# Performance work log

Measured on AMD Instinct MI355X. Metric: run time of the kernel, lower is better.

## Reference

```python
import jax, jax.numpy as jnp
import numpy as np

B, C_IN, N = 16, 64, 8192
C_OUT, NUM_RING = 128, 8
EPS = 1e-5  # BatchNorm1d default


def setup_inputs() -> dict:
    key = jax.random.key(0)
    k1, k2, k3, k4 = jax.random.split(key, 4)
    x = jax.random.normal(k1, (B, C_IN, N), dtype=jnp.float32)
    ring = jax.random.randint(k2, (B, N), 0, NUM_RING, dtype=jnp.int32)
    W = jax.random.normal(k3, (NUM_RING, C_OUT, C_IN), dtype=jnp.float32) * 0.05
    b = jax.random.normal(k4, (NUM_RING, C_OUT), dtype=jnp.float32) * 0.05
    gamma = jnp.ones((NUM_RING, C_OUT), dtype=jnp.float32)
    beta = jnp.zeros((NUM_RING, C_OUT), dtype=jnp.float32)
    return {"x": x, "ring": ring, "W": W, "b": b, "gamma": gamma, "beta": beta}


def reference(x, ring, W, b, gamma, beta):
    Bb, C, Nn = x.shape
    num_ring = W.shape[0]
    M = Bb * Nn
    xf = x.transpose(0, 2, 1).reshape(M, C)      # [M, 64] point features
    rf = ring.reshape(M)                          # [M] ring id per point

    # Per-ring Conv1d(64->128, k=1): linear with ring-selected weights.
    # num_ring is small; masked dense GEMMs avoid gathering [M,128,64] weights.
    y = jnp.zeros((M, W.shape[1]), dtype=xf.dtype)
    for r in range(num_ring):
        yr = xf @ W[r].T + b[r]
        y = jnp.where((rf == r)[:, None], yr, y)  # [M, 128]

    # Training-mode BatchNorm1d per ring group: stats over all points of that
    # ring across all batches (BN sees [1,128,M_r]). Biased variance.
    cnt = jax.ops.segment_sum(jnp.ones((M,), y.dtype), rf, num_segments=num_ring)
    cnt = jnp.maximum(cnt, 1.0)[:, None]          # [R,1]
    s = jax.ops.segment_sum(y, rf, num_segments=num_ring)       # [R,128]
    ss = jax.ops.segment_sum(y * y, rf, num_segments=num_ring)  # [R,128]
    mean = s / cnt
    var = ss / cnt - mean * mean
    yn = (y - mean[rf]) * jax.lax.rsqrt(var[rf] + EPS) * gamma[rf] + beta[rf]

    # Segment max over (batch, ring) pairs, broadcast back to every point.
    bidx = jnp.repeat(jnp.arange(Bb, dtype=rf.dtype), Nn)        # [M]
    seg = bidx * num_ring + rf
    mx = jax.ops.segment_max(yn, seg, num_segments=Bb * num_ring)  # [B*R,128]
    out = mx[seg].reshape(Bb, Nn, -1).transpose(0, 2, 1)         # [B,128,N]
    return out
```

## Files before the change

### kernel.cpp

```cpp
#include <hip/hip_runtime.h>
#include <stdint.h>
#include <math.h>

#define B_    16
#define CIN   64
#define NPT   8192
#define COUT  128
#define NRING 8
#define EPSV  1e-5f
#define CAP   2048u
#define MBLK  6

typedef unsigned int uint32;
typedef unsigned short ushort;
typedef unsigned long long ull;
typedef short short8 __attribute__((ext_vector_type(8)));
typedef float floatx4 __attribute__((ext_vector_type(4)));

__device__ __forceinline__ uint32 fkey(float f) {
  uint32 u = __float_as_uint(f);
  return (u & 0x80000000u) ? ~u : (u | 0x80000000u);
}
__device__ __forceinline__ float kinv(uint32 k) {
  uint32 u = (k & 0x80000000u) ? (k ^ 0x80000000u) : ~k;
  return __uint_as_float(u);
}
__device__ __forceinline__ uint32 f2bf(float f) {
  uint32 u = __float_as_uint(f);
  return (u + 0x7fffu + ((u >> 16) & 1u)) >> 16;
}

__global__ __launch_bounds__(256) void k_init(
    const float* __restrict__ W, ushort* __restrict__ Wb,
    uint32* __restrict__ cursor,
    float* __restrict__ sums, float* __restrict__ ssums,
    uint32* __restrict__ mxkey, uint32* __restrict__ mnkey)
{
  int tid = threadIdx.x;
  int blk = blockIdx.x;
  if (blk < 32) {
    int idx0 = blk * 256 + tid;
    for (int idx = idx0; idx < B_ * NRING * COUT; idx += 32 * 256) {
      mxkey[idx] = 0u;
      mnkey[idx] = 0xFFFFFFFFu;
      if (idx < NRING * COUT) { sums[idx] = 0.f; ssums[idx] = 0.f; }
      if (idx < B_ * NRING)   cursor[idx] = (uint32)idx * CAP;
    }
  } else {
    int idx0 = (blk - 32) * 256 + tid;
    for (int idx = idx0; idx < NRING * COUT * CIN; idx += 8 * 256)
      Wb[idx] = (ushort)f2bf(W[idx]);
  }
}

__global__ __launch_bounds__(256) void k_scatter(
    const float* __restrict__ x, const int* __restrict__ ring,
    uint32* __restrict__ cursor, ushort* __restrict__ xsb)
{
  __shared__ uint32 xl2[256 * 33];
  __shared__ int    dstrow[256];
  __shared__ ushort rankl[256];
  __shared__ uint32 wcnt[4][NRING], woff[4][NRING];
  __shared__ uint32 rbase[NRING], rstart[NRING];

  int tid  = threadIdx.x;
  int lane = tid & 63;
  int w    = tid >> 6;
  int blk  = blockIdx.x;
  int b    = blk >> 5;
  int n0   = (blk & 31) * 256;

  int rl = ring[b * NPT + n0 + tid];
  uint32 wrank = 0, mycnt = 0;
  #pragma unroll
  for (int rr = 0; rr < NRING; ++rr) {
    ull m = __ballot(rl == rr);
    if (rl == rr) wrank = (uint32)__popcll(m & ((1ull << lane) - 1ull));
    if (lane == rr) mycnt = (uint32)__popcll(m);
  }
  if (lane < NRING) wcnt[w][lane] = mycnt;
  __syncthreads();
  if (tid < NRING) {
    uint32 t = wcnt[0][tid] + wcnt[1][tid] + wcnt[2][tid] + wcnt[3][tid];
    rbase[tid] = atomicAdd(&cursor[b * NRING + tid], t);
  }
  if (tid == 0) {
    uint32 acc = 0;
    for (int rr = 0; rr < NRING; ++rr) {
      rstart[rr] = acc;
      uint32 o = acc;
      #pragma unroll
      for (int ww = 0; ww < 4; ++ww) { woff[ww][rr] = o; o += wcnt[ww][rr]; }
      acc = o;
    }
  }
  __syncthreads();
  int myrow = (int)(woff[w][rl] + wrank);
  rankl[tid] = (ushort)myrow;
  {
    uint32 gpos = rbase[rl] + ((uint32)myrow - rstart[rl]);
    uint32 limit = (uint32)(b * NRING + rl + 1) * CAP;
    dstrow[myrow] = (gpos < limit) ? (int)gpos : -1;
  }
  __syncthreads();

  int myr0 = rankl[lane * 4 + 0];
  int myr1 = rankl[lane * 4 + 1];
  int myr2 = rankl[lane * 4 + 2];
  int myr3 = rankl[lane * 4 + 3];
  const float* xb = x + (size_t)b * CIN * NPT + n0;
  #pragma unroll
  for (int kp = 0; kp < 8; ++kp) {
    int k0 = w * 16 + kp * 2;
    float4 va = *reinterpret_cast<const float4*>(xb + (size_t)k0 * NPT + lane * 4);
    float4 vb = *reinterpret_cast<const float4*>(xb + (size_t)(k0 + 1) * NPT + lane * 4);
    int idx = k0 >> 1;
    xl2[myr0 * 33 + idx] = f2bf(va.x) | (f2bf(vb.x) << 16);
    xl2[myr1 * 33 + idx] = f2bf(va.y) | (f2bf(vb.y) << 16);
    xl2[myr2 * 33 + idx] = f2bf(va.z) | (f2bf(vb.z) << 16);
    xl2[myr3 * 33 + idx] = f2bf(va.w) | (f2bf(vb.w) << 16);
  }
  __syncthreads();

  uint4* dst = reinterpret_cast<uint4*>(xsb);
  #pragma unroll
  for (int it = 0; it < 8; ++it) {
    int slot = tid + it * 256;
    int row = slot >> 3;
    int p   = slot & 7;
    int dr  = dstrow[row];
    if (dr >= 0) {
      uint4 v;
      v.x = xl2[row * 33 + 4 * p + 0];
      v.y = xl2[row * 33 + 4 * p + 1];
      v.z = xl2[row * 33 + 4 * p + 2];
      v.w = xl2[row * 33 + 4 * p + 3];
      dst[(size_t)dr * 8 + p] = v;
    }
  }
}

__global__ __launch_bounds__(256) void k_main(
    const ushort* __restrict__ xsb, const ushort* __restrict__ Wb,
    const uint32* __restrict__ cursor,
    float* __restrict__ sums, float* __restrict__ ssums,
    uint32* __restrict__ mxkey, uint32* __restrict__ mnkey)
{
  int blk = blockIdx.x;
  int c4 = blk % MBLK;
  int r  = (blk / MBLK) & 7;
  int b  = blk / (MBLK * NRING);
  uint32 segBase = (uint32)(b * NRING + r) * CAP;
  uint32 segCnt  = __builtin_amdgcn_readfirstlane(
                       min(cursor[b * NRING + r] - segBase, CAP));

  int tid = threadIdx.x;
  int lane = tid & 63;
  int w = tid >> 6;
  uint32 m0 = (uint32)(c4 * 4 + w) * 64;
  if (m0 >= segCnt) return;

  int lm = lane & 15;
  int lk = lane >> 4;

  const ushort* wr = Wb + (size_t)r * COUT * CIN;
  short8 bfr[8][2];
  #pragma unroll
  for (int nt = 0; nt < 8; ++nt) {
    const ushort* wc = wr + (size_t)(nt * 16 + lm) * CIN + lk * 8;
    bfr[nt][0] = *reinterpret_cast<const short8*>(wc);
    bfr[nt][1] = *reinterpret_cast<const short8*>(wc + 32);
  }

  float s_[8], ss_[8], mx_[8], mn_[8];
  #pragma unroll
  for (int nt = 0; nt < 8; ++nt) {
    s_[nt] = 0.f; ss_[nt] = 0.f;
    mx_[nt] = -__builtin_inff(); mn_[nt] = __builtin_inff();
  }

  #pragma unroll
  for (int mt = 0; mt < 4; ++mt) {
    uint32 row_rel = m0 + (uint32)mt * 16 + (uint32)lm;
    bool valid = row_rel < segCnt;
    uint32 row_g = segBase + (valid ? row_rel : (segCnt - 1));
    const ushort* xr = xsb + (size_t)row_g * CIN + lk * 8;
    short8 a0 = *reinterpret_cast<const short8*>(xr);
    short8 a1 = *reinterpret_cast<const short8*>(xr + 32);
    if (!valid) { a0 = (short8)0; a1 = (short8)0; }

    #pragma unroll
    for (int nt = 0; nt < 8; ++nt) {
      floatx4 f = {0.f, 0.f, 0.f, 0.f};
      f = __builtin_amdgcn_mfma_f32_16x16x32_bf16(a0, bfr[nt][0], f, 0, 0, 0);
      f = __builtin_amdgcn_mfma_f32_16x16x32_bf16(a1, bfr[nt][1], f, 0, 0, 0);
      #pragma unroll
      for (int j = 0; j < 4; ++j) {
        bool vj = (m0 + (uint32)mt * 16 + (uint32)(lk * 4 + j)) < segCnt;
        float zv = f[j];
        s_[nt] += zv;
        ss_[nt] = fmaf(zv, zv, ss_[nt]);
        mx_[nt] = fmaxf(mx_[nt], vj ? zv : -__builtin_inff());
        mn_[nt] = fminf(mn_[nt], vj ? zv :  __builtin_inff());
      }
    }
  }

  #pragma unroll
  for (int nt = 0; nt < 8; ++nt) {
    float sv = s_[nt], qv = ss_[nt], Mv = mx_[nt], mv = mn_[nt];
    sv += __shfl_xor(sv, 16, 64); sv += __shfl_xor(sv, 32, 64);
    qv += __shfl_xor(qv, 16, 64); qv += __shfl_xor(qv, 32, 64);
    Mv = fmaxf(Mv, __shfl_xor(Mv, 16, 64)); Mv = fmaxf(Mv, __shfl_xor(Mv, 32, 64));
    mv = fminf(mv, __shfl_xor(mv, 16, 64)); mv = fminf(mv, __shfl_xor(mv, 32, 64));
    if (lane < 16) {
      int ch = nt * 16 + lane;
      atomicAdd(&sums [r * COUT + ch], sv);
      atomicAdd(&ssums[r * COUT + ch], qv);
      atomicMax(&mxkey[(b * NRING + r) * COUT + ch], fkey(Mv));
      atomicMin(&mnkey[(b * NRING + r) * COUT + ch], fkey(mv));
    }
  }
}

__global__ __launch_bounds__(256) void k_bcast(
    const int* __restrict__ ring, const uint32* __restrict__ cursor,
    const float* __restrict__ sums, const float* __restrict__ ssums,
    const uint32* __restrict__ mxkey, const uint32* __restrict__ mnkey,
    const float* __restrict__ gamma, const float* __restrict__ beta,
    float* __restrict__ out)
{
  __shared__ float mxl[NRING * 129];
  __shared__ float ringcnt[NRING];
  int tid = threadIdx.x;
  int blk = blockIdx.x;
  int b   = blk >> 5;
  int n0  = (blk & 31) * 256;

  if (tid < NRING) {
    uint32 t = 0;
    for (int bb = 0; bb < B_; ++bb)
      t += min(cursor[bb * NRING + tid] - (uint32)(bb * NRING + tid) * CAP, CAP);
    ringcnt[tid] = fmaxf((float)t, 1.f);
  }
  __syncthreads();

  for (int j = tid; j < NRING * COUT; j += 256) {
    int r = j >> 7;
    float cnt  = ringcnt[r];
    float mean = sums[j] / cnt;
    float var  = fmaxf(ssums[j] / cnt - mean * mean, 0.f);
    float inv  = 1.f / sqrtf(var + EPSV);
    float a    = gamma[j] * inv;
    float bet  = beta[j];
    float zmax = kinv(mxkey[b * NRING * COUT + j]);
    float zmin = kinv(mnkey[b * NRING * COUT + j]);
    mxl[r * 129 + (j & 127)] = (a >= 0.f) ? fmaf(a, zmax - mean, bet)
                                          : fmaf(a, zmin - mean, bet);
  }
  __syncthreads();

  int wv = tid >> 6, lane = tid & 63;
  int nb = n0 + lane * 4;
  int4 r4 = *reinterpret_cast<const int4*>(&ring[b * NPT + nb]);
  int ro0 = r4.x * 129, ro1 = r4.y * 129, ro2 = r4.z * 129, ro3 = r4.w * 129;
  float* ob = out + (size_t)b * COUT * NPT + nb;
  #pragma unroll 8
  for (int c = wv * 32; c < wv * 32 + 32; ++c) {
    float4 v;
    v.x = mxl[ro0 + c];
    v.y = mxl[ro1 + c];
    v.z = mxl[ro2 + c];
    v.w = mxl[ro3 + c];
    *reinterpret_cast<float4*>(ob + (size_t)c * NPT) = v;
  }
}

extern "C" void kernel_launch(void* const* d_in, const int* in_sizes, int n_in,
                              void* d_out, int out_size, void* d_ws, size_t ws_size,
                              hipStream_t stream)
{
  const float* x     = (const float*)d_in[0];
  const int*   ring  = (const int*)  d_in[1];
  const float* W     = (const float*)d_in[2];
  const float* gamma = (const float*)d_in[4];
  const float* beta  = (const float*)d_in[5];
  float* out = (float*)d_out;

  ushort* Wb      = (ushort*)d_ws;
  uint32* cursor  = (uint32*)(Wb + 65536);
  float*  sums    = (float*)(cursor + 128);
  float*  ssums   = sums + 1024;
  uint32* mxkey   = (uint32*)(ssums + 1024);
  uint32* mnkey   = mxkey + 16384;

  ushort* xsb = (ushort*)out;

  k_init   <<<dim3(40),  dim3(256), 0, stream>>>(W, Wb, cursor, sums, ssums, mxkey, mnkey);
  k_scatter<<<dim3(512), dim3(256), 0, stream>>>(x, ring, cursor, xsb);
  k_main   <<<dim3(B_ * NRING * MBLK), dim3(256), 0, stream>>>(xsb, Wb, cursor, sums, ssums, mxkey, mnkey);
  k_bcast  <<<dim3(512), dim3(256), 0, stream>>>(ring, cursor, sums, ssums, mxkey, mnkey, gamma, beta, out);
}
```

Baseline: 77.59 us.

## Fuse scatter and per-ring GEMM into one kernel using LDS-local ring grouping

Merges the scatter and GEMM kernels: each 128-point block sorts its points by ring in LDS into 16-row padded tiles, then each wave runs the MFMA GEMM for two rings straight from LDS. This drops the global bf16 staging buffer, the per-segment cursors and their capacity cap, and one kernel launch. Statistics atomics are spread over 8 slots to reduce contention, and the broadcast kernel sums those slots. In exchange, every block reloads the weights for all rings and has padding waste in small per-ring groups, and many more atomics are issued overall.

Result: slower. 148.7 us (+91.6%).

```diff
diff --git a/kernel.cpp b/kernel.cpp
--- a/kernel.cpp
+++ b/kernel.cpp
@@ -8,8 +8,6 @@
 #define COUT  128
 #define NRING 8
 #define EPSV  1e-5f
-#define CAP   2048u
-#define MBLK  6
 
 typedef unsigned int uint32;
 typedef unsigned short ushort;
@@ -32,8 +30,8 @@
 
 __global__ __launch_bounds__(256) void k_init(
     const float* __restrict__ W, ushort* __restrict__ Wb,
-    uint32* __restrict__ cursor,
-    float* __restrict__ sums, float* __restrict__ ssums,
+    float* __restrict__ sums8, float* __restrict__ ssums8,
+    uint32* __restrict__ ringtot8,
     uint32* __restrict__ mxkey, uint32* __restrict__ mnkey)
 {
   int tid = threadIdx.x;
@@ -43,8 +41,8 @@
     for (int idx = idx0; idx < B_ * NRING * COUT; idx += 32 * 256) {
       mxkey[idx] = 0u;
       mnkey[idx] = 0xFFFFFFFFu;
-      if (idx < NRING * COUT) { sums[idx] = 0.f; ssums[idx] = 0.f; }
-      if (idx < B_ * NRING)   cursor[idx] = (uint32)idx * CAP;
+      if (idx < NRING * COUT * 8) { sums8[idx] = 0.f; ssums8[idx] = 0.f; }
+      if (idx < NRING * 8)        ringtot8[idx] = 0u;
     }
   } else {
     int idx0 = (blk - 32) * 256 + tid;
@@ -53,179 +51,149 @@
   }
 }
 
-__global__ __launch_bounds__(256) void k_scatter(
+__global__ __launch_bounds__(256, 3) void k_fused(
     const float* __restrict__ x, const int* __restrict__ ring,
-    uint32* __restrict__ cursor, ushort* __restrict__ xsb)
-{
-  __shared__ uint32 xl2[256 * 33];
-  __shared__ int    dstrow[256];
-  __shared__ ushort rankl[256];
-  __shared__ uint32 wcnt[4][NRING], woff[4][NRING];
-  __shared__ uint32 rbase[NRING], rstart[NRING];
+    const ushort* __restrict__ Wb,
+    float* __restrict__ sums8, float* __restrict__ ssums8,
+    uint32* __restrict__ ringtot8,
+    uint32* __restrict__ mxkey, uint32* __restrict__ mnkey)
+{
+  __shared__ uint32 xlf[256 * 32];
+  __shared__ ushort slotl[128];
+  __shared__ uint32 wcnt[2][NRING];
+  __shared__ uint32 gsize[NRING], astart[NRING];
 
   int tid  = threadIdx.x;
   int lane = tid & 63;
   int w    = tid >> 6;
   int blk  = blockIdx.x;
-  int b    = blk >> 5;
-  int n0   = (blk & 31) * 256;
-
-  int rl = ring[b * NPT + n0 + tid];
-  uint32 wrank = 0, mycnt = 0;
-  #pragma unroll
-  for (int rr = 0; rr < NRING; ++rr) {
-    ull m = __ballot(rl == rr);
-    if (rl == rr) wrank = (uint32)__popcll(m & ((1ull << lane) - 1ull));
-    if (lane == rr) mycnt = (uint32)__popcll(m);
-  }
-  if (lane < NRING) wcnt[w][lane] = mycnt;
-  __syncthreads();
-  if (tid < NRING) {
-    uint32 t = wcnt[0][tid] + wcnt[1][tid] + wcnt[2][tid] + wcnt[3][tid];
-    rbase[tid] = atomicAdd(&cursor[b * NRING + tid], t);
-  }
+  int b    = blk >> 6;
+  int n0   = (blk & 63) * 128;
+
+  {
+    uint4* z4 = reinterpret_cast<uint4*>(xlf);
+    #pragma unroll
+    for (int i = 0; i < 8; ++i) z4[tid + i * 256] = make_uint4(0u, 0u, 0u, 0u);
+  }
+
+  int rl = 0; uint32 wrank = 0;
+  if (tid < 128) {
+    rl = ring[b * NPT + n0 + tid];
+    #pragma unroll
+    for (int rr = 0; rr < NRING; ++rr) {
+      ull m = __ballot(rl == rr);
+      if (rl == rr) wrank = (uint32)__popcll(m & ((1ull << lane) - 1ull));
+      if (lane == rr) wcnt[w][rr] = (uint32)__popcll(m);
+    }
+  }
+  __syncthreads();
   if (tid == 0) {
-    uint32 acc = 0;
-    for (int rr = 0; rr < NRING; ++rr) {
-      rstart[rr] = acc;
-      uint32 o = acc;
-      #pragma unroll
-      for (int ww = 0; ww < 4; ++ww) { woff[ww][rr] = o; o += wcnt[ww][rr]; }
-      acc = o;
-    }
-  }
-  __syncthreads();
-  int myrow = (int)(woff[w][rl] + wrank);
-  rankl[tid] = (ushort)myrow;
+    uint32 a = 0;
+    #pragma unroll
+    for (int r = 0; r < NRING; ++r) {
+      astart[r] = a;
+      uint32 g = wcnt[0][r] + wcnt[1][r];
+      gsize[r] = g;
+      a = (a + g + 15u) & ~15u;
+    }
+  }
+  __syncthreads();
+  if (tid < 128)
+    slotl[tid] = (ushort)(astart[rl] + (w ? wcnt[0][rl] : 0u) + wrank);
+  __syncthreads();
+
   {
-    uint32 gpos = rbase[rl] + ((uint32)myrow - rstart[rl]);
-    uint32 limit = (uint32)(b * NRING + rl + 1) * CAP;
-    dstrow[myrow] = (gpos < limit) ? (int)gpos : -1;
-  }
-  __syncthreads();
-
-  int myr0 = rankl[lane * 4 + 0];
-  int myr1 = rankl[lane * 4 + 1];
-  int myr2 = rankl[lane * 4 + 2];
-  int myr3 = rankl[lane * 4 + 3];
-  const float* xb = x + (size_t)b * CIN * NPT + n0;
-  #pragma unroll
-  for (int kp = 0; kp < 8; ++kp) {
-    int k0 = w * 16 + kp * 2;
-    float4 va = *reinterpret_cast<const float4*>(xb + (size_t)k0 * NPT + lane * 4);
-    float4 vb = *reinterpret_cast<const float4*>(xb + (size_t)(k0 + 1) * NPT + lane * 4);
-    int idx = k0 >> 1;
-    xl2[myr0 * 33 + idx] = f2bf(va.x) | (f2bf(vb.x) << 16);
-    xl2[myr1 * 33 + idx] = f2bf(va.y) | (f2bf(vb.y) << 16);
-    xl2[myr2 * 33 + idx] = f2bf(va.z) | (f2bf(vb.z) << 16);
-    xl2[myr3 * 33 + idx] = f2bf(va.w) | (f2bf(vb.w) << 16);
-  }
-  __syncthreads();
-
-  uint4* dst = reinterpret_cast<uint4*>(xsb);
-  #pragma unroll
-  for (int it = 0; it < 8; ++it) {
-    int slot = tid + it * 256;
-    int row = slot >> 3;
-    int p   = slot & 7;
-    int dr  = dstrow[row];
-    if (dr >= 0) {
-      uint4 v;
-      v.x = xl2[row * 33 + 4 * p + 0];
-      v.y = xl2[row * 33 + 4 * p + 1];
-      v.z = xl2[row * 33 + 4 * p + 2];
-      v.w = xl2[row * 33 + 4 * p + 3];
-      dst[(size_t)dr * 8 + p] = v;
-    }
-  }
-}
-
-__global__ __launch_bounds__(256) void k_main(
-    const ushort* __restrict__ xsb, const ushort* __restrict__ Wb,
-    const uint32* __restrict__ cursor,
-    float* __restrict__ sums, float* __restrict__ ssums,
-    uint32* __restrict__ mxkey, uint32* __restrict__ mnkey)
-{
-  int blk = blockIdx.x;
-  int c4 = blk % MBLK;
-  int r  = (blk / MBLK) & 7;
-  int b  = blk / (MBLK * NRING);
-  uint32 segBase = (uint32)(b * NRING + r) * CAP;
-  uint32 segCnt  = __builtin_amdgcn_readfirstlane(
-                       min(cursor[b * NRING + r] - segBase, CAP));
-
-  int tid = threadIdx.x;
-  int lane = tid & 63;
-  int w = tid >> 6;
-  uint32 m0 = (uint32)(c4 * 4 + w) * 64;
-  if (m0 >= segCnt) return;
+    const float* xb = x + (size_t)b * CIN * NPT + n0;
+    int p0 = lane * 2;
+    uint32 s0 = slotl[p0], s1 = slotl[p0 + 1];
+    uint32 base0 = (s0 >> 4) * 512 + (s0 & 15) * 4;
+    uint32 base1 = (s1 >> 4) * 512 + (s1 & 15) * 4;
+    #pragma unroll
+    for (int i = 0; i < 8; ++i) {
+      int kp = w * 8 + i;
+      int k  = kp * 2;
+      float2 va = *reinterpret_cast<const float2*>(xb + (size_t)k * NPT + p0);
+      float2 vb = *reinterpret_cast<const float2*>(xb + (size_t)(k + 1) * NPT + p0);
+      uint32 off = (uint32)(kp >> 2) * 64 + (uint32)(kp & 3);
+      xlf[base0 + off] = f2bf(va.x) | (f2bf(vb.x) << 16);
+      xlf[base1 + off] = f2bf(va.y) | (f2bf(vb.y) << 16);
+    }
+  }
+  __syncthreads();
 
   int lm = lane & 15;
   int lk = lane >> 4;
-
-  const ushort* wr = Wb + (size_t)r * COUT * CIN;
-  short8 bfr[8][2];
+  int slot8 = blk & 7;
+
   #pragma unroll
-  for (int nt = 0; nt < 8; ++nt) {
-    const ushort* wc = wr + (size_t)(nt * 16 + lm) * CIN + lk * 8;
-    bfr[nt][0] = *reinterpret_cast<const short8*>(wc);
-    bfr[nt][1] = *reinterpret_cast<const short8*>(wc + 32);
-  }
-
-  float s_[8], ss_[8], mx_[8], mn_[8];
-  #pragma unroll
-  for (int nt = 0; nt < 8; ++nt) {
-    s_[nt] = 0.f; ss_[nt] = 0.f;
-    mx_[nt] = -__builtin_inff(); mn_[nt] = __builtin_inff();
-  }
-
-  #pragma unroll
-  for (int mt = 0; mt < 4; ++mt) {
-    uint32 row_rel = m0 + (uint32)mt * 16 + (uint32)lm;
-    bool valid = row_rel < segCnt;
-    uint32 row_g = segBase + (valid ? row_rel : (segCnt - 1));
-    const ushort* xr = xsb + (size_t)row_g * CIN + lk * 8;
-    short8 a0 = *reinterpret_cast<const short8*>(xr);
-    short8 a1 = *reinterpret_cast<const short8*>(xr + 32);
-    if (!valid) { a0 = (short8)0; a1 = (short8)0; }
-
+  for (int rp = 0; rp < 2; ++rp) {
+    int r = w * 2 + rp;
+    uint32 g = gsize[r];
+    if (g == 0) continue;
+
+    const ushort* wr = Wb + (size_t)r * COUT * CIN;
+    short8 bfr[8][2];
     #pragma unroll
     for (int nt = 0; nt < 8; ++nt) {
-      floatx4 f = {0.f, 0.f, 0.f, 0.f};
-      f = __builtin_amdgcn_mfma_f32_16x16x32_bf16(a0, bfr[nt][0], f, 0, 0, 0);
-      f = __builtin_amdgcn_mfma_f32_16x16x32_bf16(a1, bfr[nt][1], f, 0, 0, 0);
+      const ushort* wc = wr + (size_t)(nt * 16 + lm) * CIN + lk * 8;
+      bfr[nt][0] = *reinterpret_cast<const short8*>(wc);
+      bfr[nt][1] = *reinterpret_cast<const short8*>(wc + 32);
+    }
+
+    float s_[8], ss_[8], mx_[8], mn_[8];
+    #pragma unroll
+    for (int nt = 0; nt < 8; ++nt) {
+      s_[nt] = 0.f; ss_[nt] = 0.f;
+      mx_[nt] = -__builtin_inff(); mn_[nt] = __builtin_inff();
+    }
+
+    uint32 T = (g + 15u) >> 4;
+    uint32 tile0 = astart[r] >> 4;
+    for (uint32 t = 0; t < T; ++t) {
+      const uint32* tb = xlf + (tile0 + t) * 512;
+      short8 a0 = *reinterpret_cast<const short8*>(tb + lk * 64 + lm * 4);
+      short8 a1 = *reinterpret_cast<const short8*>(tb + (4 + lk) * 64 + lm * 4);
+
       #pragma unroll
-      for (int j = 0; j < 4; ++j) {
-        bool vj = (m0 + (uint32)mt * 16 + (uint32)(lk * 4 + j)) < segCnt;
-        float zv = f[j];
-        s_[nt] += zv;
-        ss_[nt] = fmaf(zv, zv, ss_[nt]);
-        mx_[nt] = fmaxf(mx_[nt], vj ? zv : -__builtin_inff());
-        mn_[nt] = fminf(mn_[nt], vj ? zv :  __builtin_inff());
+      for (int nt = 0; nt < 8; ++nt) {
+        floatx4 f = {0.f, 0.f, 0.f, 0.f};
+        f = __builtin_amdgcn_mfma_f32_16x16x32_bf16(a0, bfr[nt][0], f, 0, 0, 0);
+        f = __builtin_amdgcn_mfma_f32_16x16x32_bf16(a1, bfr[nt][1], f, 0, 0, 0);
+        #pragma unroll
+        for (int j = 0; j < 4; ++j) {
+          bool vj = (t * 16u + (uint32)(lk * 4 + j)) < g;
+          float zv = f[j];
+          s_[nt] += zv;
+          ss_[nt] = fmaf(zv, zv, ss_[nt]);
+          mx_[nt] = fmaxf(mx_[nt], vj ? zv : -__builtin_inff());
+          mn_[nt] = fminf(mn_[nt], vj ? zv :  __builtin_inff());
+        }
       }
     }
-  }
-
-  #pragma unroll
-  for (int nt = 0; nt < 8; ++nt) {
-    float sv = s_[nt], qv = ss_[nt], Mv = mx_[nt], mv = mn_[nt];
-    sv += __shfl_xor(sv, 16, 64); sv += __shfl_xor(sv, 32, 64);
-    qv += __shfl_xor(qv, 16, 64); qv += __shfl_xor(qv, 32, 64);
-    Mv = fmaxf(Mv, __shfl_xor(Mv, 16, 64)); Mv = fmaxf(Mv, __shfl_xor(Mv, 32, 64));
-    mv = fminf(mv, __shfl_xor(mv, 16, 64)); mv = fminf(mv, __shfl_xor(mv, 32, 64));
-    if (lane < 16) {
-      int ch = nt * 16 + lane;
-      atomicAdd(&sums [r * COUT + ch], sv);
-      atomicAdd(&ssums[r * COUT + ch], qv);
-      atomicMax(&mxkey[(b * NRING + r) * COUT + ch], fkey(Mv));
-      atomicMin(&mnkey[(b * NRING + r) * COUT + ch], fkey(mv));
-    }
+
+    #pragma unroll
+    for (int nt = 0; nt < 8; ++nt) {
+      float sv = s_[nt], qv = ss_[nt], Mv = mx_[nt], mv = mn_[nt];
+      sv += __shfl_xor(sv, 16, 64); sv += __shfl_xor(sv, 32, 64);
+      qv += __shfl_xor(qv, 16, 64); qv += __shfl_xor(qv, 32, 64);
+      Mv = fmaxf(Mv, __shfl_xor(Mv, 16, 64)); Mv = fmaxf(Mv, __shfl_xor(Mv, 32, 64));
+      mv = fminf(mv, __shfl_xor(mv, 16, 64)); mv = fminf(mv, __shfl_xor(mv, 32, 64));
+      if (lane < 16) {
+        int ch = nt * 16 + lane;
+        atomicAdd(&sums8 [(r * COUT + ch) * 8 + slot8], sv);
+        atomicAdd(&ssums8[(r * COUT + ch) * 8 + slot8], qv);
+        atomicMax(&mxkey[(b * NRING + r) * COUT + ch], fkey(Mv));
+        atomicMin(&mnkey[(b * NRING + r) * COUT + ch], fkey(mv));
+      }
+    }
+    if (lane == 0) atomicAdd(&ringtot8[r * 8 + slot8], g);
   }
 }
 
 __global__ __launch_bounds__(256) void k_bcast(
-    const int* __restrict__ ring, const uint32* __restrict__ cursor,
-    const float* __restrict__ sums, const float* __restrict__ ssums,
+    const int* __restrict__ ring,
+    const float* __restrict__ sums8, const float* __restrict__ ssums8,
+    const uint32* __restrict__ ringtot8,
     const uint32* __restrict__ mxkey, const uint32* __restrict__ mnkey,
     const float* __restrict__ gamma, const float* __restrict__ beta,
     float* __restrict__ out)
@@ -239,17 +207,20 @@
 
   if (tid < NRING) {
     uint32 t = 0;
-    for (int bb = 0; bb < B_; ++bb)
-      t += min(cursor[bb * NRING + tid] - (uint32)(bb * NRING + tid) * CAP, CAP);
+    #pragma unroll
+    for (int s = 0; s < 8; ++s) t += ringtot8[tid * 8 + s];
     ringcnt[tid] = fmaxf((float)t, 1.f);
   }
   __syncthreads();
 
   for (int j = tid; j < NRING * COUT; j += 256) {
     int r = j >> 7;
-    float cnt  = ringcnt[r];
-    float mean = sums[j] / cnt;
-    float var  = fmaxf(ssums[j] / cnt - mean * mean, 0.f);
+    float cnt = ringcnt[r];
+    float sm = 0.f, sq = 0.f;
+    #pragma unroll
+    for (int s = 0; s < 8; ++s) { sm += sums8[j * 8 + s]; sq += ssums8[j * 8 + s]; }
+    float mean = sm / cnt;
+    float var  = fmaxf(sq / cnt - mean * mean, 0.f);
     float inv  = 1.f / sqrtf(var + EPSV);
     float a    = gamma[j] * inv;
     float bet  = beta[j];
@@ -287,17 +258,14 @@
   const float* beta  = (const float*)d_in[5];
   float* out = (float*)d_out;
 
-  ushort* Wb      = (ushort*)d_ws;
-  uint32* cursor  = (uint32*)(Wb + 65536);
-  float*  sums    = (float*)(cursor + 128);
-  float*  ssums   = sums + 1024;
-  uint32* mxkey   = (uint32*)(ssums + 1024);
-  uint32* mnkey   = mxkey + 16384;
-
-  ushort* xsb = (ushort*)out;
-
-  k_init   <<<dim3(40),  dim3(256), 0, stream>>>(W, Wb, cursor, sums, ssums, mxkey, mnkey);
-  k_scatter<<<dim3(512), dim3(256), 0, stream>>>(x, ring, cursor, xsb);
-  k_main   <<<dim3(B_ * NRING * MBLK), dim3(256), 0, stream>>>(xsb, Wb, cursor, sums, ssums, mxkey, mnkey);
-  k_bcast  <<<dim3(512), dim3(256), 0, stream>>>(ring, cursor, sums, ssums, mxkey, mnkey, gamma, beta, out);
-}
+  ushort* Wb       = (ushort*)d_ws;
+  float*  sums8    = (float*)(Wb + 65536);
+  float*  ssums8   = sums8 + 8192;
+  uint32* ringtot8 = (uint32*)(ssums8 + 8192);
+  uint32* mxkey    = ringtot8 + 64;
+  uint32* mnkey    = mxkey + 16384;
+
+  k_init <<<dim3(40),   dim3(256), 0, stream>>>(W, Wb, sums8, ssums8, ringtot8, mxkey, mnkey);
+  k_fused<<<dim3(1024), dim3(256), 0, stream>>>(x, ring, Wb, sums8, ssums8, ringtot8, mxkey, mnkey);
+  k_bcast<<<dim3(512),  dim3(256), 0, stream>>>(ring, sums8, ssums8, ringtot8, mxkey, mnkey, gamma, beta, out);
+}
```
